# Kernel optimization log

Hardware: AMD Instinct MI355X
Metric: run time of the kernel (lower is better)

Reference implementation:

```python
import jax, jax.numpy as jnp
import numpy as np

N = 100000   # nodes per node type ('net' and 'cell')
E = 600000   # edges per canonical relation
D_IN = 16    # raw input feature dim
D = 128      # hidden dim (in_size == out_size, required by wl: Linear(2*D -> D))
SLOPE = 0.2  # DGL GATConv leaky_relu negative slope


def setup_inputs() -> dict:
    key = jax.random.key(0)
    ks = jax.random.split(key, 24)
    f = lambda k, shp, scale=1.0: jax.random.normal(k, shp, dtype=jnp.float32) * scale
    s_in = 1.0 / np.sqrt(D_IN).astype(np.float32)
    s_d = 1.0 / np.sqrt(D).astype(np.float32)
    s_2d = 1.0 / np.sqrt(2 * D).astype(np.float32)
    inp = {
        'x_net':   f(ks[0], (N, D_IN)),
        'x_cell':  f(ks[1], (N, D_IN)),
        'Wp_net':  f(ks[2], (D, D_IN), s_in),
        'Wp_cell': f(ks[3], (D, D_IN), s_in),
        # per-edge-type GATConv params: fc weight + attn_l + attn_r (num_heads=1, no bias)
        'Wg0': f(ks[4], (D, D), s_d), 'al0': f(ks[5], (D,), s_d), 'ar0': f(ks[6], (D,), s_d),
        'Wg1': f(ks[7], (D, D), s_d), 'al1': f(ks[8], (D,), s_d), 'ar1': f(ks[9], (D,), s_d),
        'Wg2': f(ks[10], (D, D), s_d), 'al2': f(ks[11], (D,), s_d), 'ar2': f(ks[12], (D,), s_d),
        'Wl':   f(ks[13], (D, 2 * D), s_2d),
        'bias': jnp.zeros((D,), jnp.float32),
        # edge lists: relation 0 = cell->net, 1 = net->cell, 2 = net->net
        'src0': jax.random.randint(ks[14], (E,), 0, N, dtype=jnp.int32),
        'dst0': jax.random.randint(ks[15], (E,), 0, N, dtype=jnp.int32),
        'src1': jax.random.randint(ks[16], (E,), 0, N, dtype=jnp.int32),
        'dst1': jax.random.randint(ks[17], (E,), 0, N, dtype=jnp.int32),
        'src2': jax.random.randint(ks[18], (E,), 0, N, dtype=jnp.int32),
        'dst2': jax.random.randint(ks[19], (E,), 0, N, dtype=jnp.int32),
    }
    return inp


def _gat(x_src, x_dst, W, al, ar, src, dst):
    """DGL GATConv (num_heads=1, bias=False) on one relation's edge list."""
    h_src = x_src @ W.T                               # [N, D]
    h_dst = x_dst @ W.T                               # [N, D]
    el = (h_src @ al)[src]                            # [E] gathered src logits
    er = (h_dst @ ar)[dst]                            # [E] gathered dst logits
    e = jax.nn.leaky_relu(el + er, SLOPE)             # [E]
    # segment softmax over incoming edges of each dst node
    m = jax.ops.segment_max(e, dst, num_segments=N)
    ex = jnp.exp(e - m[dst])
    denom = jax.ops.segment_sum(ex, dst, num_segments=N)
    alpha = ex / denom[dst]                           # [E]
    return jax.ops.segment_sum(h_src[src] * alpha[:, None], dst, num_segments=N)


def reference(x_net, x_cell, Wp_net, Wp_cell,
              Wg0, al0, ar0, Wg1, al1, ar1, Wg2, al2, ar2,
              Wl, bias,
              src0, dst0, src1, dst1, src2, dst2):
    # feature projection per node type (ParaGraph.feat_proj)
    h_net = x_net @ Wp_net.T                          # [N, D]
    h_cell = x_cell @ Wp_cell.T                       # [N, D]
    feat = {'net': h_net, 'cell': h_cell}
    out = {'net': jnp.zeros((N, D), h_net.dtype), 'cell': jnp.zeros((N, D), h_cell.dtype)}
    # canonical etypes: (srctype, dsttype, gat params, edge list)
    rels = [
        ('cell', 'net', Wg0, al0, ar0, src0, dst0),
        ('net', 'cell', Wg1, al1, ar1, src1, dst1),
        ('net', 'net',  Wg2, al2, ar2, src2, dst2),
    ]
    for st, dt, W, al, ar, src, dst in rels:
        out[dt] = out[dt] + _gat(feat[st], feat[dt], W, al, ar, src, dst)
        # faithful to the original: concat+linear+relu recomputed for EVERY ntype
        # inside the etype loop (the redundant fused-op pattern)
        for nt in ('net', 'cell'):
            out[nt] = jax.nn.relu(
                jnp.concatenate([feat[nt], out[nt] + bias], axis=1) @ Wl.T)
    return jnp.stack([out['net'], out['cell']])      # [2, N, D]
```

## Files before the change

kernel.cpp:

```cpp
#include <hip/hip_runtime.h>
#include <hip/hip_bf16.h>
#include <stdint.h>

#define NN 100000
#define NE 600000
#define SP 136
#define NB 782
#define BCAP 1600
#define CHUNK 4096
#define NCH 147
#define GB 1563
#define AB 6250

typedef unsigned short u16;
typedef unsigned int u32;
typedef __attribute__((ext_vector_type(8))) short short8;
typedef __attribute__((ext_vector_type(8))) __bf16 bf16x8;
typedef __attribute__((ext_vector_type(4))) float floatx4;

__device__ __forceinline__ float b2f(u16 u) {
  union { float f; u32 i; } c; c.i = ((u32)u) << 16; return c.f;
}
__device__ __forceinline__ u16 f2b(float f) {
  union { float f; u32 i; } c; c.f = f;
  u32 r = c.i + 0x7FFFu + ((c.i >> 16) & 1u);
  return (u16)(r >> 16);
}


__device__ __forceinline__ void gemm_w(const u16* __restrict__ W, int ldw, u16* __restrict__ C,
                                       u16* lds, int tid, int row0, const bf16x8* a,
                                       int m16, int quad, int wv) {
#pragma unroll
  for (int it = 0; it < 8; ++it) {
    int idx = it * 256 + tid;
    int r = idx >> 4, c = (idx & 15) << 3;
    *(short8*)(&lds[r * SP + c]) = *(const short8*)(W + (size_t)r * ldw + c);
  }
  __syncthreads();
  const u16* brow = &lds[m16 * SP + quad * 8];
  floatx4 acc[8];
#pragma unroll
  for (int c = 0; c < 8; ++c) acc[c] = floatx4{0.f, 0.f, 0.f, 0.f};
#pragma unroll
  for (int kk = 0; kk < 4; ++kk) {
#pragma unroll
    for (int c = 0; c < 8; ++c) {
      bf16x8 bfr = *(const bf16x8*)(brow + c * 16 * SP + kk * 32);
      acc[c] = __builtin_amdgcn_mfma_f32_16x16x32_bf16(a[kk], bfr, acc[c], 0, 0, 0);
    }
  }
#pragma unroll
  for (int c = 0; c < 8; ++c) {
    int col = c * 16 + m16;
#pragma unroll
    for (int r = 0; r < 4; ++r) {
      int grow = row0 + wv * 16 + quad * 4 + r;
      if (grow < NN) C[(size_t)grow * 128 + col] = f2b(acc[c][r]);
    }
  }
}

template<int FINAL>
__device__ __forceinline__ void fused_body(int blk, int tid, const u16* __restrict__ A,
                                           const u16* __restrict__ P, void* __restrict__ C,
                                           const u16* __restrict__ W, const float* __restrict__ cvec,
                                           u16* Wlds) {
  const int row0 = blk * 64;
#pragma unroll
  for (int it = 0; it < 8; ++it) {
    int idx = it * 256 + tid;
    int r = idx >> 4, c = (idx & 15) << 3;
    *(short8*)(&Wlds[r * SP + c]) = *(const short8*)(W + (size_t)r * 256 + c);
  }
  const int lane = tid & 63, wv = tid >> 6;
  const int m16 = lane & 15, quad = lane >> 4;
  int arow = row0 + wv * 16 + m16;
  if (arow >= NN) arow = NN - 1;
  const u16* Ab = A + (size_t)arow * 128 + quad * 8;
  bf16x8 a[4];
#pragma unroll
  for (int kk = 0; kk < 4; ++kk) a[kk] = *(const bf16x8*)(Ab + kk * 32);
  __syncthreads();
  const u16* brow = &Wlds[m16 * SP + quad * 8];
  floatx4 acc[8];
#pragma unroll
  for (int c = 0; c < 8; ++c) acc[c] = floatx4{0.f, 0.f, 0.f, 0.f};
#pragma unroll
  for (int kk = 0; kk < 4; ++kk) {
#pragma unroll
    for (int c = 0; c < 8; ++c) {
      bf16x8 bfr = *(const bf16x8*)(brow + c * 16 * SP + kk * 32);
      acc[c] = __builtin_amdgcn_mfma_f32_16x16x32_bf16(a[kk], bfr, acc[c], 0, 0, 0);
    }
  }
#pragma unroll
  for (int c = 0; c < 8; ++c) {
    int col = c * 16 + m16;
    float cv = cvec[col];
#pragma unroll
    for (int r = 0; r < 4; ++r) {
      int grow = row0 + wv * 16 + quad * 4 + r;
      if (grow < NN) {
        float v = acc[c][r] + b2f(P[(size_t)grow * 128 + col]) + cv;
        v = fmaxf(v, 0.f);
        if (FINAL) ((float*)C)[(size_t)grow * 128 + col] = v;
        else       ((u16*)C)[(size_t)grow * 128 + col] = f2b(v);
      }
    }
  }
}

template<int RMW, int FINAL>
__device__ __forceinline__ void aggF_body(int nb, int tid,
                                          const u16* __restrict__ h, const u32* __restrict__ srecs,
                                          const int* __restrict__ rp,
                                          const float* __restrict__ el, const float* __restrict__ er,
                                          const u16* __restrict__ prevbuf,
                                          const u16* __restrict__ P, const float* __restrict__ cvec,
                                          const u16* __restrict__ W,
                                          void* __restrict__ out,
                                          u16* Wlds, u16* Alds) {
#pragma unroll
  for (int it = 0; it < 8; ++it) {
    int idx = it * 256 + tid;
    int r = idx >> 4, c = (idx & 15) << 3;
    *(short8*)(&Wlds[r * SP + c]) = *(const short8*)(W + (size_t)r * 256 + c);
  }
  int sub = tid & 15;
  int g = tid >> 4;
  int n = nb * 16 + g;
  int start = rp[n], end = rp[n + 1];
  float row[8];
  if (RMW) {
    short8 pv = *(const short8*)(prevbuf + (size_t)n * 128 + sub * 8);
#pragma unroll
    for (int t = 0; t < 8; ++t) row[t] = b2f((u16)pv[t]);
  } else {
#pragma unroll
    for (int t = 0; t < 8; ++t) row[t] = 0.f;
  }
  if (start < end) {
    float ern = er[n];
    float acc[8];
#pragma unroll
    for (int t = 0; t < 8; ++t) acc[t] = 0.f;
    float sl = 0.f;
    const u16* hsub = h + sub * 8;
    for (int base = start; base < end; base += 16) {
      int m = end - base; if (m > 16) m = 16;
      int srci = 0; float w = 0.f;
      if (sub < m) {
        srci = (int)srecs[base + sub];
        float l = el[srci] + ern;
        l = (l >= 0.f) ? l : 0.2f * l;
        w = __expf(l);
      }
      sl += w;
      for (int i = 0; i < m; ++i) {
        float x = __shfl(w, i, 16);
        int sv = __shfl(srci, i, 16);
        short8 hv = *(const short8*)(hsub + (size_t)sv * 128);
#pragma unroll
        for (int t = 0; t < 8; ++t) acc[t] += x * b2f((u16)hv[t]);
      }
    }
    float s = sl;
#pragma unroll
    for (int off = 8; off > 0; off >>= 1) s += __shfl_xor(s, off, 16);
    float inv = 1.f / s;
#pragma unroll
    for (int t = 0; t < 8; ++t) row[t] += acc[t] * inv;
  }
  short8 rb;
#pragma unroll
  for (int t = 0; t < 8; ++t) rb[t] = (short)f2b(row[t]);
  *(short8*)(&Alds[g * SP + sub * 8]) = rb;
  __syncthreads();
  const int lane = tid & 63, wv = tid >> 6;
  const int m16 = lane & 15, quad = lane >> 4;
  const u16* arow = &Alds[m16 * SP + quad * 8];
  bf16x8 a[4];
#pragma unroll
  for (int kk = 0; kk < 4; ++kk) a[kk] = *(const bf16x8*)(arow + kk * 32);
  const u16* brow = &Wlds[m16 * SP + quad * 8];
  floatx4 acc2[2];
#pragma unroll
  for (int cc = 0; cc < 2; ++cc) acc2[cc] = floatx4{0.f, 0.f, 0.f, 0.f};
#pragma unroll
  for (int kk = 0; kk < 4; ++kk) {
#pragma unroll
    for (int cc = 0; cc < 2; ++cc) {
      int ct = wv * 2 + cc;
      bf16x8 bfr = *(const bf16x8*)(brow + ct * 16 * SP + kk * 32);
      acc2[cc] = __builtin_amdgcn_mfma_f32_16x16x32_bf16(a[kk], bfr, acc2[cc], 0, 0, 0);
    }
  }
#pragma unroll
  for (int cc = 0; cc < 2; ++cc) {
    int ct = wv * 2 + cc;
    int col = ct * 16 + m16;
    float cv = cvec[col];
#pragma unroll
    for (int r = 0; r < 4; ++r) {
      int node = nb * 16 + quad * 4 + r;
      float v = acc2[cc][r] + b2f(P[(size_t)node * 128 + col]) + cv;
      v = fmaxf(v, 0.f);
      if (FINAL) ((float*)out)[(size_t)node * 128 + col] = v;
      else       ((u16*)out)[(size_t)node * 128 + col] = f2b(v);
    }
  }
}


__global__ __launch_bounds__(256) void prep_k(const float* __restrict__ x_net, const float* __restrict__ x_cell,
                                              const float* __restrict__ Wp_net, const float* __restrict__ Wp_cell,
                                              u16* __restrict__ feat_net, u16* __restrict__ feat_cell,
                                              const float* __restrict__ Wl, const float* __restrict__ Wg0,
                                              const float* __restrict__ Wg1, const float* __restrict__ Wg2,
                                              u16* __restrict__ Wl_bf, u16* __restrict__ Wg_bf,
                                              const float* al0, const float* ar0, const float* al1,
                                              const float* ar1, const float* al2, const float* ar2,
                                              const float* bias, float* __restrict__ vecs,
                                              int* __restrict__ bcnt) {
  int bid = blockIdx.x, tid = threadIdx.x;
  if (bid < 2 * AB) {
    int y = bid >= AB;
    int bx = y ? bid - AB : bid;
    const float* x  = y ? x_cell : x_net;
    const float* Wp = y ? Wp_cell : Wp_net;
    u16* feat       = y ? feat_cell : feat_net;
    __shared__ float Ws[128 * 17];
    __shared__ float xs[16][17];
#pragma unroll
    for (int it = 0; it < 8; ++it) {
      int idx = it * 256 + tid;
      int j = idx >> 4, k = idx & 15;
      Ws[j * 17 + k] = Wp[idx];
    }
    int n0 = bx * 16;
    { int nn = tid >> 4, k = tid & 15;
      xs[nn][k] = x[(size_t)(n0 + nn) * 16 + k]; }
    __syncthreads();
    int j = tid & 127, g = tid >> 7;
    float acc[8];
#pragma unroll
    for (int r = 0; r < 8; ++r) acc[r] = 0.f;
#pragma unroll
    for (int k = 0; k < 16; ++k) {
      float w = Ws[j * 17 + k];
#pragma unroll
      for (int r = 0; r < 8; ++r) acc[r] += xs[g * 8 + r][k] * w;
    }
#pragma unroll
    for (int r = 0; r < 8; ++r)
      feat[(size_t)(n0 + g * 8 + r) * 128 + j] = f2b(acc[r]);
  } else if (bid < 2 * AB + 128) {
    int cid = bid - 2 * AB;
    int y = cid >> 5, bx = cid & 31;
    const float* src = (y == 0) ? Wl : (y == 1) ? Wg0 : (y == 2) ? Wg1 : Wg2;
    u16* dst = (y == 0) ? Wl_bf : Wg_bf + (size_t)(y - 1) * 16384;
    int n = (y == 0) ? 32768 : 16384;
    int i = (bx * 256 + tid) * 4;
    if (i >= n) return;
    float4 v = *(const float4*)(src + i);
    ushort4 p; p.x = f2b(v.x); p.y = f2b(v.y); p.z = f2b(v.z); p.w = f2b(v.w);
    *(ushort4*)(dst + i) = p;
  } else if (bid < 2 * AB + 135) {
    int a = bid - (2 * AB + 128);
    if (tid >= 128) return;
    int j = tid;
    float s = 0.f;
    if (a < 6) {
      const float* W = (a < 2) ? Wg0 : (a < 4) ? Wg1 : Wg2;
      const float* v = (a == 0) ? al0 : (a == 1) ? ar0 : (a == 2) ? al1 : (a == 3) ? ar1 : (a == 4) ? al2 : ar2;
      for (int i = 0; i < 128; ++i) s += W[i * 128 + j] * v[i];
    } else {
      for (int i = 0; i < 128; ++i) s += Wl[(size_t)j * 256 + 128 + i] * bias[i];
    }
    vecs[a * 128 + j] = s;
  } else {
    int r = bid - (2 * AB + 135);
    for (int i = tid; i < NB; i += 256) bcnt[(size_t)r * NB + i] = 0;
  }
}

__global__ __launch_bounds__(256) void logbh_k(const u16* __restrict__ feat_net, const u16* __restrict__ feat_cell,
                                               const float* __restrict__ vecs, float* __restrict__ outs,
                                               const int* __restrict__ dst0, const int* __restrict__ dst1,
                                               const int* __restrict__ dst2, int* __restrict__ bcnt) {
  __shared__ int sm[NB];
  int bid = blockIdx.x, tid = threadIdx.x;
  if (bid < 782) {
    float* vs = (float*)sm;
#pragma unroll
    for (int it = 0; it < 3; ++it) vs[it * 256 + tid] = vecs[it * 256 + tid];
    __syncthreads();
    int y = bid >= 391;
    int bx = y ? bid - 391 : bid;
    const u16* f = y ? feat_cell : feat_net;
    int n = bx * 256 + tid;
    if (n >= NN) return;
    const u16* row = f + (size_t)n * 128;
    if (y == 0) {
      float s1 = 0.f, s2 = 0.f, s4 = 0.f, s5 = 0.f;
#pragma unroll
      for (int k = 0; k < 128; k += 8) {
        short8 u = *(const short8*)(row + k);
#pragma unroll
        for (int t = 0; t < 8; ++t) {
          float fv = b2f((u16)u[t]);
          s1 += fv * vs[1 * 128 + k + t]; s2 += fv * vs[2 * 128 + k + t];
          s4 += fv * vs[4 * 128 + k + t]; s5 += fv * vs[5 * 128 + k + t];
        }
      }
      outs[(size_t)1 * NN + n] = s1; outs[(size_t)2 * NN + n] = s2;
      outs[(size_t)4 * NN + n] = s4; outs[(size_t)5 * NN + n] = s5;
    } else {
      float s0 = 0.f, s3 = 0.f;
#pragma unroll
      for (int k = 0; k < 128; k += 8) {
        short8 u = *(const short8*)(row + k);
#pragma unroll
        for (int t = 0; t < 8; ++t) {
          float fv = b2f((u16)u[t]);
          s0 += fv * vs[0 * 128 + k + t]; s3 += fv * vs[3 * 128 + k + t];
        }
      }
      outs[(size_t)0 * NN + n] = s0; outs[(size_t)3 * NN + n] = s3;
    }
  } else {
    int e = bid - 782;
    int r = e / NCH, bx = e % NCH;
    const int* dst = (r == 0) ? dst0 : (r == 1) ? dst1 : dst2;
    for (int i = tid; i < NB; i += 256) sm[i] = 0;
    __syncthreads();
    int e0 = bx * CHUNK;
    int cnt = NE - e0; if (cnt > CHUNK) cnt = CHUNK;
    for (int i = tid; i < cnt; i += 256) atomicAdd(&sm[((u32)dst[e0 + i]) >> 7], 1);
    __syncthreads();
    for (int b = tid; b < NB; b += 256) {
      int c = sm[b];
      if (c) atomicAdd(&bcnt[(size_t)r * NB + b], c);
    }
  }
}

__global__ __launch_bounds__(1024) void bscan_k(const int* __restrict__ bcnt, int* __restrict__ bptr,
                                                int* __restrict__ bcur) {
  int r = blockIdx.x, t = threadIdx.x;
  const int* c = bcnt + (size_t)r * NB;
  int* p = bptr + (size_t)r * (NB + 1);
  int* cur = bcur + (size_t)r * NB;
  int v = (t < NB) ? c[t] : 0;
  __shared__ int ss[1024];
  ss[t] = v; __syncthreads();
  for (int off = 1; off < 1024; off <<= 1) {
    int u = (t >= off) ? ss[t - off] : 0;
    __syncthreads();
    ss[t] += u;
    __syncthreads();
  }
  if (t < NB) { int e = ss[t] - v; p[t] = e; cur[t] = e; }
  if (t == 1023) p[NB] = ss[1023];
}

__global__ __launch_bounds__(256) void bscatter_k(const int* __restrict__ src0, const int* __restrict__ dst0,
                                                  const int* __restrict__ src1, const int* __restrict__ dst1,
                                                  const int* __restrict__ src2, const int* __restrict__ dst2,
                                                  int* __restrict__ bcur, u32* __restrict__ recs) {
  int r = blockIdx.y;
  const int* src = (r == 0) ? src0 : (r == 1) ? src1 : src2;
  const int* dst = (r == 0) ? dst0 : (r == 1) ? dst1 : dst2;
  __shared__ int hist[NB];
  __shared__ int lstart[NB];
  __shared__ int lcur[NB];
  __shared__ int badj[NB];
  __shared__ u32 rbuf[CHUNK];
  __shared__ u16 kbuf[CHUNK];
  __shared__ int ss[256];
  int tid = threadIdx.x;
  int e0 = blockIdx.x * CHUNK;
  int cnt = NE - e0; if (cnt > CHUNK) cnt = CHUNK;

  for (int i = tid; i < NB; i += 256) hist[i] = 0;
  __syncthreads();
  for (int i = tid; i < cnt; i += 256) atomicAdd(&hist[((u32)dst[e0 + i]) >> 7], 1);
  __syncthreads();
  int loc[4]; int s = 0;
  int base4 = tid * 4;
#pragma unroll
  for (int j = 0; j < 4; ++j) {
    int idx = base4 + j;
    int v = (idx < NB) ? hist[idx] : 0;
    loc[j] = s; s += v;
  }
  ss[tid] = s; __syncthreads();
  for (int off = 1; off < 256; off <<= 1) {
    int u = (tid >= off) ? ss[tid - off] : 0;
    __syncthreads();
    ss[tid] += u;
    __syncthreads();
  }
  int ex = ss[tid] - s;
#pragma unroll
  for (int j = 0; j < 4; ++j) {
    int idx = base4 + j;
    if (idx < NB) { int e = ex + loc[j]; lstart[idx] = e; lcur[idx] = e; }
  }
  __syncthreads();
  for (int b = tid; b < NB; b += 256) {
    int c = hist[b];
    int g = 0;
    if (c) g = atomicAdd(&bcur[(size_t)r * NB + b], c);
    badj[b] = g - lstart[b];
  }
  __syncthreads();
  for (int i = tid; i < cnt; i += 256) {
    int dN = dst[e0 + i], sN = src[e0 + i];
    int b = ((u32)dN) >> 7;
    int pos = atomicAdd(&lcur[b], 1);
    rbuf[pos] = ((u32)(dN & 127) << 17) | (u32)sN;
    kbuf[pos] = (u16)b;
  }
  __syncthreads();
  u32* out = recs + (size_t)r * NE;
  for (int i = tid; i < cnt; i += 256) {
    int b = kbuf[i];
    out[badj[b] + i] = rbuf[i];
  }
}

__global__ __launch_bounds__(256) void sortgemm_k(u32* __restrict__ recs, const int* __restrict__ bptr,
                                                  int* __restrict__ rowptr,
                                                  const u16* __restrict__ feat_net, const u16* __restrict__ feat_cell,
                                                  const u16* __restrict__ Wl_bf, const u16* __restrict__ Wg_bf,
                                                  u16* __restrict__ P_net, u16* __restrict__ P_cell,
                                                  u16* __restrict__ h0, u16* __restrict__ h1, u16* __restrict__ h2) {
  __shared__ u32 smem[128 * SP / 2];
  int bid = blockIdx.x, tid = threadIdx.x;
  if (bid < 2 * GB) {
    int ntype = bid >= GB;
    int blk = ntype ? bid - GB : bid;
    u16* lds = (u16*)smem;
    const u16* A = ntype ? feat_cell : feat_net;
    const int row0 = blk * 64;
    const int lane = tid & 63, wv = tid >> 6;
    const int m16 = lane & 15, quad = lane >> 4;
    int arow = row0 + wv * 16 + m16;
    if (arow >= NN) arow = NN - 1;
    const u16* Ab = A + (size_t)arow * 128 + quad * 8;
    bf16x8 a[4];
#pragma unroll
    for (int kk = 0; kk < 4; ++kk) a[kk] = *(const bf16x8*)(Ab + kk * 32);
    if (!ntype) {
      gemm_w(Wl_bf,          256, P_net, lds, tid, row0, a, m16, quad, wv);
      __syncthreads();
      gemm_w(Wg_bf + 16384,  128, h1,    lds, tid, row0, a, m16, quad, wv);
      __syncthreads();
      gemm_w(Wg_bf + 32768,  128, h2,    lds, tid, row0, a, m16, quad, wv);
    } else {
      gemm_w(Wl_bf,          256, P_cell, lds, tid, row0, a, m16, quad, wv);
      __syncthreads();
      gemm_w(Wg_bf,          128, h0,     lds, tid, row0, a, m16, quad, wv);
    }
  } else {
    int sb = bid - 2 * GB;
    int r = sb / NB, b = sb % NB;
    const int* p = bptr + (size_t)r * (NB + 1);
    u32* rec = recs + (size_t)r * NE;
    int* rp = rowptr + (size_t)r * (NN + 1);
    int base = p[b], end = p[b + 1];
    int cnt = end - base; if (cnt > BCAP) cnt = BCAP;
    u32* rs = smem;
    int* hist = (int*)(smem + BCAP);
    int* excl = hist + 128;
    int* cur  = excl + 128;
    for (int i = tid; i < cnt; i += 256) rs[i] = rec[base + i];
    if (tid < 128) hist[tid] = 0;
    __syncthreads();
    for (int i = tid; i < cnt; i += 256) atomicAdd(&hist[rs[i] >> 17], 1);
    __syncthreads();
    if (tid < 128) cur[tid] = hist[tid];
    __syncthreads();
    for (int off = 1; off < 128; off <<= 1) {
      int v = 0;
      if (tid < 128 && tid >= off) v = cur[tid - off];
      __syncthreads();
      if (tid < 128) cur[tid] += v;
      __syncthreads();
    }
    if (tid < 128) {
      int e = cur[tid] - hist[tid];
      excl[tid] = e;
      int node = b * 128 + tid;
      if (node < NN) rp[node] = base + e;
    }
    if (b == NB - 1 && tid == 0) rp[NN] = p[NB];
    if (tid < 128) cur[tid] = excl[tid];
    __syncthreads();
    for (int i = tid; i < cnt; i += 256) {
      u32 v = rs[i];
      int pos = atomicAdd(&cur[v >> 17], 1);
      rec[base + pos] = v & 0x1FFFFu;
    }
  }
}

__global__ __launch_bounds__(256) void aggelem_k(const u16* __restrict__ h0, const u32* __restrict__ srecs,
                                                 const int* __restrict__ rp,
                                                 const float* __restrict__ el, const float* __restrict__ er,
                                                 const u16* __restrict__ P_net, const float* __restrict__ cvec,
                                                 const u16* __restrict__ W2, u16* __restrict__ buf_net,
                                                 const u16* __restrict__ P_cell, u16* __restrict__ buf_cell) {
  __shared__ u16 Wlds[128 * SP];
  __shared__ u16 Alds[16 * SP];
  int bid = blockIdx.x, tid = threadIdx.x;
  if (bid < AB) {
    aggF_body<0, 0>(bid, tid, h0, srecs, rp, el, er, nullptr, P_net, cvec, W2,
                    (void*)buf_net, Wlds, Alds);
  } else {
    float* cs = (float*)Alds;
    int bx = bid - AB;
    if (tid < 128) cs[tid] = cvec[tid];
    __syncthreads();
    size_t idx = ((size_t)bx * 256 + tid) * 8;
    if (idx >= (size_t)NN * 128) return;
    int col = (int)(idx & 127);
    short8 u = *(const short8*)(P_cell + idx);
    short8 w;
#pragma unroll
    for (int t = 0; t < 8; ++t)
      w[t] = (short)f2b(fmaxf(b2f((u16)u[t]) + cs[col + t], 0.f));
    *(short8*)(buf_cell + idx) = w;
  }
}

__global__ __launch_bounds__(256) void aggfused1_k(const u16* __restrict__ h1, const u32* __restrict__ srecs,
                                                   const int* __restrict__ rp,
                                                   const float* __restrict__ el, const float* __restrict__ er,
                                                   const u16* __restrict__ P_cell, u16* __restrict__ buf_cell,
                                                   const u16* __restrict__ buf_net, const u16* __restrict__ P_net,
                                                   u16* __restrict__ buf_net_out,
                                                   const u16* __restrict__ W2, const float* __restrict__ cvec) {
  __shared__ u16 Wlds[128 * SP];
  __shared__ u16 Alds[16 * SP];
  int bid = blockIdx.x, tid = threadIdx.x;
  if (bid < AB) {
    aggF_body<1, 0>(bid, tid, h1, srecs, rp, el, er, buf_cell, P_cell, cvec, W2,
                    (void*)buf_cell, Wlds, Alds);
  } else {
    fused_body<0>(bid - AB, tid, buf_net, P_net, (void*)buf_net_out, W2, cvec, Wlds);
  }
}

__global__ __launch_bounds__(256) void aggfused2_k(const u16* __restrict__ h2, const u32* __restrict__ srecs,
                                                   const int* __restrict__ rp,
                                                   const float* __restrict__ el, const float* __restrict__ er,
                                                   const u16* __restrict__ buf_net, const u16* __restrict__ P_net,
                                                   float* __restrict__ out_net,
                                                   const u16* __restrict__ buf_cell, const u16* __restrict__ P_cell,
                                                   float* __restrict__ out_cell,
                                                   const u16* __restrict__ W2, const float* __restrict__ cvec) {
  __shared__ u16 Wlds[128 * SP];
  __shared__ u16 Alds[16 * SP];
  int bid = blockIdx.x, tid = threadIdx.x;
  if (bid < AB) {
    aggF_body<1, 1>(bid, tid, h2, srecs, rp, el, er, buf_net, P_net, cvec, W2,
                    (void*)out_net, Wlds, Alds);
  } else {
    fused_body<1>(bid - AB, tid, buf_cell, P_cell, (void*)out_cell, W2, cvec, Wlds);
  }
}

extern "C" void kernel_launch(void* const* d_in, const int* in_sizes, int n_in,
                              void* d_out, int out_size, void* d_ws, size_t ws_size,
                              hipStream_t stream) {
  const float* x_net   = (const float*)d_in[0];
  const float* x_cell  = (const float*)d_in[1];
  const float* Wp_net  = (const float*)d_in[2];
  const float* Wp_cell = (const float*)d_in[3];
  const float* Wg[3] = {(const float*)d_in[4], (const float*)d_in[7], (const float*)d_in[10]};
  const float* al[3] = {(const float*)d_in[5], (const float*)d_in[8], (const float*)d_in[11]};
  const float* ar[3] = {(const float*)d_in[6], (const float*)d_in[9], (const float*)d_in[12]};
  const float* Wl    = (const float*)d_in[13];
  const float* bias  = (const float*)d_in[14];
  const int* src[3] = {(const int*)d_in[15], (const int*)d_in[17], (const int*)d_in[19]};
  const int* dst[3] = {(const int*)d_in[16], (const int*)d_in[18], (const int*)d_in[20]};

  char* ws = (char*)d_ws;
  size_t off = 0;
  auto alloc = [&](size_t b) { void* p = ws + off; off = (off + b + 255) & ~(size_t)255; return p; };
  u16*  feat_net  = (u16*)alloc((size_t)NN * 128 * 2);
  u16*  feat_cell = (u16*)alloc((size_t)NN * 128 * 2);
  u16*  hbuf0     = (u16*)alloc((size_t)NN * 128 * 2);
  u16*  hbuf1     = (u16*)alloc((size_t)NN * 128 * 2);
  u16*  hbuf2     = (u16*)alloc((size_t)NN * 128 * 2);
  u16*  P_net     = (u16*)alloc((size_t)NN * 128 * 2);
  u16*  P_cell    = (u16*)alloc((size_t)NN * 128 * 2);
  u16*  buf_net   = (u16*)alloc((size_t)NN * 128 * 2);
  u16*  buf_cell  = (u16*)alloc((size_t)NN * 128 * 2);
  float* vecs     = (float*)alloc(7 * 128 * 4);
  float* logit    = (float*)alloc((size_t)6 * NN * 4);
  u16*   Wl_bf    = (u16*)alloc((size_t)128 * 256 * 2);
  u16*   Wg_bf    = (u16*)alloc((size_t)3 * 128 * 128 * 2);
  int*   bcnt     = (int*)alloc((size_t)3 * NB * 4);
  int*   bcur     = (int*)alloc((size_t)3 * NB * 4);
  int*   bptr     = (int*)alloc((size_t)3 * (NB + 1) * 4);
  int*   rowptr   = (int*)alloc((size_t)3 * (NN + 1) * 4);
  u32*   recs     = (u32*)alloc((size_t)3 * NE * 4);

  float* out_f = (float*)d_out;
  const u16* W2 = Wl_bf + 128;
  const float* cvec = vecs + 6 * 128;

  prep_k<<<2 * AB + 138, 256, 0, stream>>>(x_net, x_cell, Wp_net, Wp_cell, feat_net, feat_cell,
                                           Wl, Wg[0], Wg[1], Wg[2], Wl_bf, Wg_bf,
                                           al[0], ar[0], al[1], ar[1], al[2], ar[2], bias, vecs, bcnt);
  logbh_k<<<782 + 3 * NCH, 256, 0, stream>>>(feat_net, feat_cell, vecs, logit,
                                             dst[0], dst[1], dst[2], bcnt);
  bscan_k<<<3, 1024, 0, stream>>>(bcnt, bptr, bcur);
  bscatter_k<<<dim3(NCH, 3), 256, 0, stream>>>(src[0], dst[0], src[1], dst[1], src[2], dst[2],
                                               bcur, recs);
  sortgemm_k<<<2 * GB + 3 * NB, 256, 0, stream>>>(recs, bptr, rowptr, feat_net, feat_cell,
                                                  Wl_bf, Wg_bf, P_net, P_cell, hbuf0, hbuf1, hbuf2);
  aggelem_k<<<2 * AB, 256, 0, stream>>>(hbuf0, recs, rowptr, logit, logit + (size_t)NN,
                                        P_net, cvec, W2, buf_net, P_cell, buf_cell);
  aggfused1_k<<<AB + GB, 256, 0, stream>>>(hbuf1, recs + (size_t)NE, rowptr + (NN + 1),
                                           logit + (size_t)2 * NN, logit + (size_t)3 * NN,
                                           P_cell, buf_cell, buf_net, P_net, buf_net, W2, cvec);
  aggfused2_k<<<AB + GB, 256, 0, stream>>>(hbuf2, recs + (size_t)2 * NE, rowptr + 2 * (NN + 1),
                                           logit + (size_t)4 * NN, logit + (size_t)5 * NN,
                                           buf_net, P_net, out_f,
                                           buf_cell, P_cell, out_f + (size_t)NN * 128, W2, cvec);
}
```

Baseline: 469.9 us.

## Fuse three tail aggregation kernels into one per-node-block kernel keeping rows in LDS

```diff
diff --git a/kernel.cpp b/kernel.cpp
--- a/kernel.cpp
+++ b/kernel.cpp
@@ -61,79 +61,26 @@
   }
 }
 
-template<int FINAL>
-__device__ __forceinline__ void fused_body(int blk, int tid, const u16* __restrict__ A,
-                                           const u16* __restrict__ P, void* __restrict__ C,
-                                           const u16* __restrict__ W, const float* __restrict__ cvec,
-                                           u16* Wlds) {
-  const int row0 = blk * 64;
+__device__ __forceinline__ void stageW2(const u16* __restrict__ W2, u16* Wlds, int tid) {
 #pragma unroll
   for (int it = 0; it < 8; ++it) {
     int idx = it * 256 + tid;
     int r = idx >> 4, c = (idx & 15) << 3;
-    *(short8*)(&Wlds[r * SP + c]) = *(const short8*)(W + (size_t)r * 256 + c);
-  }
-  const int lane = tid & 63, wv = tid >> 6;
-  const int m16 = lane & 15, quad = lane >> 4;
-  int arow = row0 + wv * 16 + m16;
-  if (arow >= NN) arow = NN - 1;
-  const u16* Ab = A + (size_t)arow * 128 + quad * 8;
-  bf16x8 a[4];
-#pragma unroll
-  for (int kk = 0; kk < 4; ++kk) a[kk] = *(const bf16x8*)(Ab + kk * 32);
-  __syncthreads();
-  const u16* brow = &Wlds[m16 * SP + quad * 8];
-  floatx4 acc[8];
-#pragma unroll
-  for (int c = 0; c < 8; ++c) acc[c] = floatx4{0.f, 0.f, 0.f, 0.f};
-#pragma unroll
-  for (int kk = 0; kk < 4; ++kk) {
-#pragma unroll
-    for (int c = 0; c < 8; ++c) {
-      bf16x8 bfr = *(const bf16x8*)(brow + c * 16 * SP + kk * 32);
-      acc[c] = __builtin_amdgcn_mfma_f32_16x16x32_bf16(a[kk], bfr, acc[c], 0, 0, 0);
-    }
-  }
-#pragma unroll
-  for (int c = 0; c < 8; ++c) {
-    int col = c * 16 + m16;
-    float cv = cvec[col];
-#pragma unroll
-    for (int r = 0; r < 4; ++r) {
-      int grow = row0 + wv * 16 + quad * 4 + r;
-      if (grow < NN) {
-        float v = acc[c][r] + b2f(P[(size_t)grow * 128 + col]) + cv;
-        v = fmaxf(v, 0.f);
-        if (FINAL) ((float*)C)[(size_t)grow * 128 + col] = v;
-        else       ((u16*)C)[(size_t)grow * 128 + col] = f2b(v);
-      }
-    }
-  }
-}
-
-template<int RMW, int FINAL>
-__device__ __forceinline__ void aggF_body(int nb, int tid,
-                                          const u16* __restrict__ h, const u32* __restrict__ srecs,
-                                          const int* __restrict__ rp,
+    *(short8*)(&Wlds[r * SP + c]) = *(const short8*)(W2 + (size_t)r * 256 + c);
+  }
+}
+
+template<int INIT>
+__device__ __forceinline__ void gat_phase(int nb, int tid, const u16* __restrict__ h,
+                                          const u32* __restrict__ srecs, const int* __restrict__ rp,
                                           const float* __restrict__ el, const float* __restrict__ er,
-                                          const u16* __restrict__ prevbuf,
-                                          const u16* __restrict__ P, const float* __restrict__ cvec,
-                                          const u16* __restrict__ W,
-                                          void* __restrict__ out,
-                                          u16* Wlds, u16* Alds) {
-#pragma unroll
-  for (int it = 0; it < 8; ++it) {
-    int idx = it * 256 + tid;
-    int r = idx >> 4, c = (idx & 15) << 3;
-    *(short8*)(&Wlds[r * SP + c]) = *(const short8*)(W + (size_t)r * 256 + c);
-  }
-  int sub = tid & 15;
-  int g = tid >> 4;
+                                          u16* Alds) {
+  int sub = tid & 15, g = tid >> 4;
   int n = nb * 16 + g;
   int start = rp[n], end = rp[n + 1];
   float row[8];
-  if (RMW) {
-    short8 pv = *(const short8*)(prevbuf + (size_t)n * 128 + sub * 8);
+  if (INIT) {
+    short8 pv = *(const short8*)(&Alds[g * SP + sub * 8]);
 #pragma unroll
     for (int t = 0; t < 8; ++t) row[t] = b2f((u16)pv[t]);
   } else {
@@ -176,13 +123,19 @@
 #pragma unroll
   for (int t = 0; t < 8; ++t) rb[t] = (short)f2b(row[t]);
   *(short8*)(&Alds[g * SP + sub * 8]) = rb;
-  __syncthreads();
+}
+
+template<int TO_GLOBAL>
+__device__ __forceinline__ void F_phase(int nb, int tid, const u16* __restrict__ P,
+                                        const float* __restrict__ cvec,
+                                        const u16* Wlds, u16* Alds, void* __restrict__ out) {
   const int lane = tid & 63, wv = tid >> 6;
   const int m16 = lane & 15, quad = lane >> 4;
   const u16* arow = &Alds[m16 * SP + quad * 8];
   bf16x8 a[4];
 #pragma unroll
   for (int kk = 0; kk < 4; ++kk) a[kk] = *(const bf16x8*)(arow + kk * 32);
+  if (!TO_GLOBAL) __syncthreads();
   const u16* brow = &Wlds[m16 * SP + quad * 8];
   floatx4 acc2[2];
 #pragma unroll
@@ -203,13 +156,15 @@
     float cv = cvec[col];
 #pragma unroll
     for (int r = 0; r < 4; ++r) {
-      int node = nb * 16 + quad * 4 + r;
+      int nrow = quad * 4 + r;
+      int node = nb * 16 + nrow;
       float v = acc2[cc][r] + b2f(P[(size_t)node * 128 + col]) + cv;
       v = fmaxf(v, 0.f);
-      if (FINAL) ((float*)out)[(size_t)node * 128 + col] = v;
-      else       ((u16*)out)[(size_t)node * 128 + col] = f2b(v);
-    }
-  }
+      if (TO_GLOBAL) ((float*)out)[(size_t)node * 128 + col] = v;
+      else           Alds[nrow * SP + col] = f2b(v);
+    }
+  }
+  if (!TO_GLOBAL) __syncthreads();
 }
 
 
@@ -507,69 +462,44 @@
   }
 }
 
-__global__ __launch_bounds__(256) void aggelem_k(const u16* __restrict__ h0, const u32* __restrict__ srecs,
-                                                 const int* __restrict__ rp,
-                                                 const float* __restrict__ el, const float* __restrict__ er,
-                                                 const u16* __restrict__ P_net, const float* __restrict__ cvec,
-                                                 const u16* __restrict__ W2, u16* __restrict__ buf_net,
-                                                 const u16* __restrict__ P_cell, u16* __restrict__ buf_cell) {
+__global__ __launch_bounds__(256) void tail_k(const u16* __restrict__ h0, const u16* __restrict__ h1,
+                                              const u16* __restrict__ h2,
+                                              const u32* __restrict__ recs, const int* __restrict__ rowptr,
+                                              const float* __restrict__ logit,
+                                              const u16* __restrict__ P_net, const u16* __restrict__ P_cell,
+                                              const u16* __restrict__ W2, const float* __restrict__ cvec,
+                                              float* __restrict__ out_net, float* __restrict__ out_cell) {
   __shared__ u16 Wlds[128 * SP];
   __shared__ u16 Alds[16 * SP];
   int bid = blockIdx.x, tid = threadIdx.x;
+  stageW2(W2, Wlds, tid);
   if (bid < AB) {
-    aggF_body<0, 0>(bid, tid, h0, srecs, rp, el, er, nullptr, P_net, cvec, W2,
-                    (void*)buf_net, Wlds, Alds);
+    int nb = bid;
+    gat_phase<0>(nb, tid, h0, recs, rowptr, logit, logit + (size_t)NN, Alds);
+    __syncthreads();
+    F_phase<0>(nb, tid, P_net, cvec, Wlds, Alds, nullptr);
+    F_phase<0>(nb, tid, P_net, cvec, Wlds, Alds, nullptr);
+    gat_phase<1>(nb, tid, h2, recs + (size_t)2 * NE, rowptr + 2 * (NN + 1),
+                 logit + (size_t)4 * NN, logit + (size_t)5 * NN, Alds);
+    __syncthreads();
+    F_phase<1>(nb, tid, P_net, cvec, Wlds, Alds, (void*)out_net);
   } else {
-    float* cs = (float*)Alds;
-    int bx = bid - AB;
-    if (tid < 128) cs[tid] = cvec[tid];
-    __syncthreads();
-    size_t idx = ((size_t)bx * 256 + tid) * 8;
-    if (idx >= (size_t)NN * 128) return;
-    int col = (int)(idx & 127);
-    short8 u = *(const short8*)(P_cell + idx);
-    short8 w;
-#pragma unroll
-    for (int t = 0; t < 8; ++t)
-      w[t] = (short)f2b(fmaxf(b2f((u16)u[t]) + cs[col + t], 0.f));
-    *(short8*)(buf_cell + idx) = w;
-  }
-}
-
-__global__ __launch_bounds__(256) void aggfused1_k(const u16* __restrict__ h1, const u32* __restrict__ srecs,
-                                                   const int* __restrict__ rp,
-                                                   const float* __restrict__ el, const float* __restrict__ er,
-                                                   const u16* __restrict__ P_cell, u16* __restrict__ buf_cell,
-                                                   const u16* __restrict__ buf_net, const u16* __restrict__ P_net,
-                                                   u16* __restrict__ buf_net_out,
-                                                   const u16* __restrict__ W2, const float* __restrict__ cvec) {
-  __shared__ u16 Wlds[128 * SP];
-  __shared__ u16 Alds[16 * SP];
-  int bid = blockIdx.x, tid = threadIdx.x;
-  if (bid < AB) {
-    aggF_body<1, 0>(bid, tid, h1, srecs, rp, el, er, buf_cell, P_cell, cvec, W2,
-                    (void*)buf_cell, Wlds, Alds);
-  } else {
-    fused_body<0>(bid - AB, tid, buf_net, P_net, (void*)buf_net_out, W2, cvec, Wlds);
-  }
-}
-
-__global__ __launch_bounds__(256) void aggfused2_k(const u16* __restrict__ h2, const u32* __restrict__ srecs,
-                                                   const int* __restrict__ rp,
-                                                   const float* __restrict__ el, const float* __restrict__ er,
-                                                   const u16* __restrict__ buf_net, const u16* __restrict__ P_net,
-                                                   float* __restrict__ out_net,
-                                                   const u16* __restrict__ buf_cell, const u16* __restrict__ P_cell,
-                                                   float* __restrict__ out_cell,
-                                                   const u16* __restrict__ W2, const float* __restrict__ cvec) {
-  __shared__ u16 Wlds[128 * SP];
-  __shared__ u16 Alds[16 * SP];
-  int bid = blockIdx.x, tid = threadIdx.x;
-  if (bid < AB) {
-    aggF_body<1, 1>(bid, tid, h2, srecs, rp, el, er, buf_net, P_net, cvec, W2,
-                    (void*)out_net, Wlds, Alds);
-  } else {
-    fused_body<1>(bid - AB, tid, buf_cell, P_cell, (void*)out_cell, W2, cvec, Wlds);
+    int nb = bid - AB;
+    {
+      int sub = tid & 15, g = tid >> 4;
+      int n = nb * 16 + g;
+      short8 pv = *(const short8*)(P_cell + (size_t)n * 128 + sub * 8);
+      short8 rb;
+#pragma unroll
+      for (int t = 0; t < 8; ++t)
+        rb[t] = (short)f2b(fmaxf(b2f((u16)pv[t]) + cvec[sub * 8 + t], 0.f));
+      *(short8*)(&Alds[g * SP + sub * 8]) = rb;
+    }
+    gat_phase<1>(nb, tid, h1, recs + (size_t)NE, rowptr + (NN + 1),
+                 logit + (size_t)2 * NN, logit + (size_t)3 * NN, Alds);
+    __syncthreads();
+    F_phase<0>(nb, tid, P_cell, cvec, Wlds, Alds, nullptr);
+    F_phase<1>(nb, tid, P_cell, cvec, Wlds, Alds, (void*)out_cell);
   }
 }
 
@@ -598,8 +528,6 @@
   u16*  hbuf2     = (u16*)alloc((size_t)NN * 128 * 2);
   u16*  P_net     = (u16*)alloc((size_t)NN * 128 * 2);
   u16*  P_cell    = (u16*)alloc((size_t)NN * 128 * 2);
-  u16*  buf_net   = (u16*)alloc((size_t)NN * 128 * 2);
-  u16*  buf_cell  = (u16*)alloc((size_t)NN * 128 * 2);
   float* vecs     = (float*)alloc(7 * 128 * 4);
   float* logit    = (float*)alloc((size_t)6 * NN * 4);
   u16*   Wl_bf    = (u16*)alloc((size_t)128 * 256 * 2);
@@ -624,13 +552,7 @@
                                                bcur, recs);
   sortgemm_k<<<2 * GB + 3 * NB, 256, 0, stream>>>(recs, bptr, rowptr, feat_net, feat_cell,
                                                   Wl_bf, Wg_bf, P_net, P_cell, hbuf0, hbuf1, hbuf2);
-  aggelem_k<<<2 * AB, 256, 0, stream>>>(hbuf0, recs, rowptr, logit, logit + (size_t)NN,
-                                        P_net, cvec, W2, buf_net, P_cell, buf_cell);
-  aggfused1_k<<<AB + GB, 256, 0, stream>>>(hbuf1, recs + (size_t)NE, rowptr + (NN + 1),
-                                           logit + (size_t)2 * NN, logit + (size_t)3 * NN,
-                                           P_cell, buf_cell, buf_net, P_net, buf_net, W2, cvec);
-  aggfused2_k<<<AB + GB, 256, 0, stream>>>(hbuf2, recs + (size_t)2 * NE, rowptr + 2 * (NN + 1),
-                                           logit + (size_t)4 * NN, logit + (size_t)5 * NN,
-                                           buf_net, P_net, out_f,
-                                           buf_cell, P_cell, out_f + (size_t)NN * 128, W2, cvec);
-}
+  tail_k<<<2 * AB, 256, 0, stream>>>(hbuf0, hbuf1, hbuf2, recs, rowptr, logit,
+                                     P_net, P_cell, W2, cvec,
+                                     out_f, out_f + (size_t)NN * 128);
+}
```

Measured after the change: 433.6 us. 7.7% less time.
